# Performance work log

Measured on AMD Instinct MI355X. Metric: run time of the kernel, lower is better.

The kernel has to match this reference:

```python
import jax, jax.numpy as jnp
import numpy as np
import math

# ---- static configuration (mirrors Renderer defaults) ----
S = 129                                 # density cube side
L = math.ceil(S * math.sqrt(3))         # padded/rotation cube side = 224
C_ABS = 0.2                             # absorption coefficient c
LIGHTS = [
    {'dir': (2, 1, 1),    'rgb': (1.0, 69.0 / 255.0, 25.0 / 255.0)},
    {'dir': (-1, 0.5, 0), 'rgb': (227.0 / 255.0, 1.0, 66.0 / 255.0)},
]


def yp_from_light(l):
    ld = np.asarray(l, dtype=np.float64)
    ld = ld / np.sqrt(np.sum(ld ** 2))
    y = -math.asin(ld[0])
    if ld[2] < 0:
        y = -math.pi - y
    y = y * 180.0 / math.pi
    p = math.asin(ld[1]) * 180.0 / math.pi
    return y, p


def rot_matrix(yaw_deg, pitch_deg, order):
    # yaw about the y (height) axis, pitch about the x axis, roll = 0
    y = math.radians(yaw_deg)
    p = math.radians(pitch_deg)
    Ry = np.array([[math.cos(y), 0.0, math.sin(y)],
                   [0.0, 1.0, 0.0],
                   [-math.sin(y), 0.0, math.cos(y)]], dtype=np.float32)
    Rp = np.array([[1.0, 0.0, 0.0],
                   [0.0, math.cos(p), -math.sin(p)],
                   [0.0, math.sin(p), math.cos(p)]], dtype=np.float32)
    return Ry @ Rp if order == 'ypr' else Rp @ Ry

# base normalized sampling grid (align_corners=True convention), (x,y,z) order
_lin = np.linspace(-1.0, 1.0, L, dtype=np.float32)
_zz, _yy, _xx = np.meshgrid(_lin, _lin, _lin, indexing='ij')
BASE_XYZ = np.stack([_xx, _yy, _zz], axis=-1)   # [L,L,L,3]


def rotate_volume(vol, R):
    """Trilinear resampling of vol [B,C,D,H,W] under rotation R (zero padding)."""
    B, Ch, D, H, W = vol.shape
    src = jnp.einsum('dhwc,kc->dhwk', jnp.asarray(BASE_XYZ), jnp.asarray(R))
    xs = (src[..., 0] + 1.0) * 0.5 * (W - 1)
    ys = (src[..., 1] + 1.0) * 0.5 * (H - 1)
    zs = (src[..., 2] + 1.0) * 0.5 * (D - 1)
    x0 = jnp.floor(xs).astype(jnp.int32)
    y0 = jnp.floor(ys).astype(jnp.int32)
    z0 = jnp.floor(zs).astype(jnp.int32)
    wx = (xs - x0).astype(vol.dtype)
    wy = (ys - y0).astype(vol.dtype)
    wz = (zs - z0).astype(vol.dtype)
    flat = vol.reshape(B, Ch, D * H * W)

    def gather(zi, yi, xi):
        inb = ((zi >= 0) & (zi < D) & (yi >= 0) & (yi < H) & (xi >= 0) & (xi < W)).astype(vol.dtype)
        idx = ((jnp.clip(zi, 0, D - 1) * H + jnp.clip(yi, 0, H - 1)) * W
               + jnp.clip(xi, 0, W - 1)).reshape(-1)
        return jnp.take(flat, idx, axis=2).reshape(B, Ch, D, H, W) * inb

    out = (gather(z0,     y0,     x0)     * ((1 - wz) * (1 - wy) * (1 - wx))
         + gather(z0,     y0,     x0 + 1) * ((1 - wz) * (1 - wy) * wx)
         + gather(z0,     y0 + 1, x0)     * ((1 - wz) * wy * (1 - wx))
         + gather(z0,     y0 + 1, x0 + 1) * ((1 - wz) * wy * wx)
         + gather(z0 + 1, y0,     x0)     * (wz * (1 - wy) * (1 - wx))
         + gather(z0 + 1, y0,     x0 + 1) * (wz * (1 - wy) * wx)
         + gather(z0 + 1, y0 + 1, x0)     * (wz * wy * (1 - wx))
         + gather(z0 + 1, y0 + 1, x0 + 1) * (wz * wy * wx))
    return out


def _revcumsum(a):
    # torch.flip(cumsum(flip(a,[2]),2),[2]) : reverse cumulative sum along depth
    return jnp.flip(jnp.cumsum(jnp.flip(a, 2), axis=2), 2)


def setup_inputs() -> dict:
    key = jax.random.key(0)
    d = jax.random.uniform(key, (1, 1, S, S, S), dtype=jnp.float32)
    return {'d': d}


def reference(d):
    bs, _, Sd, _, _ = d.shape
    i = L // 2 - Sd // 2
    j = i + Sd
    light_array = jnp.zeros((bs, 3, Sd, Sd, Sd), dtype=d.dtype)
    for l in LIGHTS:
        y, p = yp_from_light(l['dir'])
        up = jnp.zeros((bs, 1, L, L, L), dtype=d.dtype).at[:, :, i:j, i:j, i:j].set(d)
        up = rotate_volume(up, rot_matrix(y, p, 'ypr'))
        up = jnp.exp(-C_ABS * _revcumsum(up))           # transmittance toward light
        up = rotate_volume(up, rot_matrix(-y, -p, 'rpy'))
        color = jnp.asarray(l['rgb'], dtype=d.dtype).reshape(1, 3, 1, 1, 1)
        light_array = light_array + up[:, :, i:j, i:j, i:j] * color
    t = jnp.exp(-C_ABS * _revcumsum(d))                  # view-ray transmittance
    out = C_ABS * jnp.sum(d * light_array * t, axis=2)   # background = 0
    return jnp.clip(out, 0.0, 1.0)
```

## Files before the change

kernel.cpp:

```cpp
#include <hip/hip_runtime.h>
#include <hip/hip_fp16.h>
#include <math.h>

#ifndef M_PI
#define M_PI 3.14159265358979323846
#endif

#define SS   129
#define LL   224
#define LL2  (LL*LL)
#define LL3  (LL*LL*LL)
#define SS2  (SS*SS)
#define SS3  (SS*SS*SS)
#define CABS 0.2f
#define PAD  48

#define BLO 45.5f
#define BHI 178.5f

#define NT1  28
#define NTZ16 14
#define ROTG  (2 * NTZ16 * 784)
#define NT3  17
#define NBZ16 9
#define BACKG (2 * NBZ16 * 289)
#define NTZ  28
#define NSEG 4
#define SEGZ 33
#define CVTB 8386

#define RBX 21
#define RBY 16
#define RBZ 18
#define RBN (RBX*RBY*RBZ)
#define RSXZ (RBX*RBZ)

#define BBX 21
#define BBY 16
#define BBZ 19
#define BBN (BBX*BBY*BBZ)
#define BSXZ (BBX*BBZ)

struct Mat3 { float m[9]; };
struct F3   { float x, y, z; };

__device__ __forceinline__ F3 tile_center(const Mat3& M, int ox, int oy, int oz) {
    float cbx = fmaf((float)ox + 3.5f, 2.0f / 223.0f, -1.0f);
    float cby = fmaf((float)oy + 3.5f, 2.0f / 223.0f, -1.0f);
    float cbz = fmaf((float)oz + 3.5f, 2.0f / 223.0f, -1.0f);
    F3 qc;
    qc.x = fmaf(fmaf(M.m[0], cbx, fmaf(M.m[1], cby, M.m[2] * cbz)), 111.5f, 111.5f);
    qc.y = fmaf(fmaf(M.m[3], cbx, fmaf(M.m[4], cby, M.m[5] * cbz)), 111.5f, 111.5f);
    qc.z = fmaf(fmaf(M.m[6], cbx, fmaf(M.m[7], cby, M.m[8] * cbz)), 111.5f, 111.5f);
    return qc;
}

__device__ __forceinline__ F3 tile_center16(const Mat3& M, int ox, int oy, int oz) {
    float cbx = fmaf((float)ox + 3.5f, 2.0f / 223.0f, -1.0f);
    float cby = fmaf((float)oy + 3.5f, 2.0f / 223.0f, -1.0f);
    float cbz = fmaf((float)oz + 7.5f, 2.0f / 223.0f, -1.0f);
    F3 qc;
    qc.x = fmaf(fmaf(M.m[0], cbx, fmaf(M.m[1], cby, M.m[2] * cbz)), 111.5f, 111.5f);
    qc.y = fmaf(fmaf(M.m[3], cbx, fmaf(M.m[4], cby, M.m[5] * cbz)), 111.5f, 111.5f);
    qc.z = fmaf(fmaf(M.m[6], cbx, fmaf(M.m[7], cby, M.m[8] * cbz)), 111.5f, 111.5f);
    return qc;
}

__device__ __forceinline__ bool tile_accept(F3 qc, F3 H) {
    return !(qc.x + H.x < BLO || qc.x - H.x > BHI ||
             qc.y + H.y < BLO || qc.y - H.y > BHI ||
             qc.z + H.z < BLO || qc.z - H.z > BHI);
}

__device__ __forceinline__ void qmap(const Mat3& M, int x, int y, int z,
                                     float& qx, float& qy, float& qz) {
    float bx = fmaf((float)x, 2.0f / 223.0f, -1.0f);
    float by = fmaf((float)y, 2.0f / 223.0f, -1.0f);
    float bz = fmaf((float)z, 2.0f / 223.0f, -1.0f);
    qx = fmaf(fmaf(M.m[0], bx, fmaf(M.m[1], by, M.m[2] * bz)), 111.5f, 111.5f);
    qy = fmaf(fmaf(M.m[3], bx, fmaf(M.m[4], by, M.m[5] * bz)), 111.5f, 111.5f);
    qz = fmaf(fmaf(M.m[6], bx, fmaf(M.m[7], by, M.m[8] * bz)), 111.5f, 111.5f);
}

__device__ __forceinline__ float fetch_d(const float* __restrict__ d, int z, int y, int x) {
    unsigned zz = (unsigned)(z - PAD), yy = (unsigned)(y - PAD), xx = (unsigned)(x - PAD);
    return (zz < (unsigned)SS && yy < (unsigned)SS && xx < (unsigned)SS)
        ? d[((int)zz * SS + (int)yy) * SS + (int)xx] : 0.0f;
}

__device__ __forceinline__ float fetch_d16(const __half* __restrict__ d, int z, int y, int x) {
    unsigned zz = (unsigned)(z - PAD), yy = (unsigned)(y - PAD), xx = (unsigned)(x - PAD);
    return (zz < (unsigned)SS && yy < (unsigned)SS && xx < (unsigned)SS)
        ? __half2float(d[((int)zz * SS + (int)yy) * SS + (int)xx]) : 0.0f;
}

__device__ __forceinline__ float fetch_T(const float* __restrict__ T, int z, int y, int x) {
    unsigned zz = (unsigned)z, yy = (unsigned)y, xx = (unsigned)x;
    return (zz < (unsigned)LL && yy < (unsigned)LL && xx < (unsigned)LL)
        ? T[((int)zz * LL + (int)yy) * LL + (int)xx] : 0.0f;
}

__device__ __forceinline__ float tri_T(const float* __restrict__ T, float qz, float qy, float qx) {
    int x0 = (int)floorf(qx), y0 = (int)floorf(qy), z0 = (int)floorf(qz);
    float wx = qx - (float)x0, wy = qy - (float)y0, wz = qz - (float)z0;
    float c000 = fetch_T(T, z0, y0, x0),     c001 = fetch_T(T, z0, y0, x0 + 1);
    float c010 = fetch_T(T, z0, y0 + 1, x0), c011 = fetch_T(T, z0, y0 + 1, x0 + 1);
    float c100 = fetch_T(T, z0 + 1, y0, x0),     c101 = fetch_T(T, z0 + 1, y0, x0 + 1);
    float c110 = fetch_T(T, z0 + 1, y0 + 1, x0), c111 = fetch_T(T, z0 + 1, y0 + 1, x0 + 1);
    float a00 = c000 + wx * (c001 - c000), a01 = c010 + wx * (c011 - c010);
    float a10 = c100 + wx * (c101 - c100), a11 = c110 + wx * (c111 - c110);
    float b0 = a00 + wy * (a01 - a00), b1 = a10 + wy * (a11 - a10);
    return b0 + wz * (b1 - b0);
}

__device__ __forceinline__ float tri_d_g(const float* __restrict__ d, float qz, float qy, float qx) {
    int x0 = (int)floorf(qx), y0 = (int)floorf(qy), z0 = (int)floorf(qz);
    float wx = qx - (float)x0, wy = qy - (float)y0, wz = qz - (float)z0;
    float c000 = fetch_d(d, z0, y0, x0),     c001 = fetch_d(d, z0, y0, x0 + 1);
    float c010 = fetch_d(d, z0, y0 + 1, x0), c011 = fetch_d(d, z0, y0 + 1, x0 + 1);
    float c100 = fetch_d(d, z0 + 1, y0, x0),     c101 = fetch_d(d, z0 + 1, y0, x0 + 1);
    float c110 = fetch_d(d, z0 + 1, y0 + 1, x0), c111 = fetch_d(d, z0 + 1, y0 + 1, x0 + 1);
    float a00 = c000 + wx * (c001 - c000), a01 = c010 + wx * (c011 - c010);
    float a10 = c100 + wx * (c101 - c100), a11 = c110 + wx * (c111 - c110);
    float b0 = a00 + wy * (a01 - a00), b1 = a10 + wy * (a11 - a10);
    return b0 + wz * (b1 - b0);
}

__device__ __forceinline__ float tri_rot(const float* __restrict__ S,
                                         float qx, float qy, float qz,
                                         int lox, int loy, int loz) {
    int x0 = (int)floorf(qx), y0 = (int)floorf(qy), z0 = (int)floorf(qz);
    float wx = qx - (float)x0, wy = qy - (float)y0, wz = qz - (float)z0;
    int i = (y0 - loy) * 378 + (z0 - loz) * 21 + (x0 - lox);
    float c000 = S[i],        c001 = S[i + 1];
    float cz0  = S[i + 21],   cz1  = S[i + 22];
    float cy0  = S[i + 378],  cy1  = S[i + 379];
    float cw0  = S[i + 399],  cw1  = S[i + 400];
    float a00 = c000 + wx * (c001 - c000);
    float a01 = cy0  + wx * (cy1  - cy0);
    float a10 = cz0  + wx * (cz1  - cz0);
    float a11 = cw0  + wx * (cw1  - cw0);
    float b0  = a00 + wy * (a01 - a00);
    float b1  = a10 + wy * (a11 - a10);
    return b0 + wz * (b1 - b0);
}

__device__ __forceinline__ float tri_back(const float* __restrict__ S,
                                          float qx, float qy, float qz,
                                          int lox, int loy, int loz) {
    int x0 = (int)floorf(qx), y0 = (int)floorf(qy), z0 = (int)floorf(qz);
    float wx = qx - (float)x0, wy = qy - (float)y0, wz = qz - (float)z0;
    int i = (y0 - loy) * 399 + (z0 - loz) * 21 + (x0 - lox);
    float c000 = S[i],        c001 = S[i + 1];
    float cz0  = S[i + 21],   cz1  = S[i + 22];
    float cy0  = S[i + 399],  cy1  = S[i + 400];
    float cw0  = S[i + 420],  cw1  = S[i + 421];
    float a00 = c000 + wx * (c001 - c000);
    float a01 = cy0  + wx * (cy1  - cy0);
    float a10 = cz0  + wx * (cz1  - cz0);
    float a11 = cw0  + wx * (cw1  - cw0);
    float b0  = a00 + wy * (a01 - a00);
    float b1  = a10 + wy * (a11 - a10);
    return b0 + wz * (b1 - b0);
}

__global__ __launch_bounds__(256) void k_pre(const float* __restrict__ d,
        float* __restrict__ Dseg, float* __restrict__ A,
        unsigned short* __restrict__ Run, __half* __restrict__ d16,
        Mat3 M0, Mat3 M1, F3 H0, F3 H1) {
    int b = blockIdx.x;
    if (b < 261) {
        int t = b * 256 + threadIdx.x;
        if (t < 2 * SS2) A[t] = 0.0f;
        if (t >= NSEG * SS2) return;
        int seg = t / SS2, col = t - seg * SS2;
        int zs = seg * SEGZ, ze = min(SS, zs + SEGZ);
        float run = 0.0f;
        for (int z = zs; z < ze; ++z) run += d[z * SS2 + col];
        Dseg[t] = run;
    } else if (b < 268) {
        int id = (b - 261) * 256 + threadIdx.x;
        if (id >= 2 * 784) return;
        int l = id / 784, r = id - l * 784;
        int ty = r / 28, tx = r - ty * 28;
        const Mat3 M = l ? M1 : M0;
        const F3  H  = l ? H1 : H0;
        int t0 = -1, t1 = -1;
        for (int tz = 0; tz < NT1; ++tz) {
            F3 qc = tile_center(M, tx * 8, ty * 8, tz * 8);
            if (tile_accept(qc, H)) { if (t0 < 0) t0 = tz; t1 = tz; }
        }
        Run[id] = (t0 < 0) ? 0xFFFFu : (unsigned short)(t0 | (t1 << 8));
    } else {
        int t = (b - 268) * 256 + threadIdx.x;
        if (t < SS3) d16[t] = __float2half(d[t]);
    }
}

__global__ __launch_bounds__(512) void k_rot(const __half* __restrict__ d16,
        __half* __restrict__ T0, __half* __restrict__ T1,
        float* __restrict__ S0, float* __restrict__ S1,
        const unsigned short* __restrict__ Run,
        Mat3 M0, Mat3 M1, F3 H0, F3 H1) {
    int b = blockIdx.x;
    int light = b / (NTZ16 * 784);
    int r = b - light * (NTZ16 * 784);
    int tz16 = r / 784;
    int r2 = r - tz16 * 784;
    int tty = r2 / 28, ttx = r2 - tty * 28;

    unsigned short rt = Run[light * 784 + tty * 28 + ttx];
    if (rt == 0xFFFFu) return;
    int t0 = rt & 0xFF, t1 = rt >> 8;
    if (2 * tz16 + 1 < t0 || 2 * tz16 > t1) return;

    const Mat3 M = light ? M1 : M0;
    const F3  H  = light ? H1 : H0;
    __half* __restrict__ T   = light ? T1 : T0;
    float* __restrict__ Ssum = light ? S1 : S0;

    int ox = ttx * 8, oy = tty * 8, oz = tz16 * 16;
    F3 qc = tile_center16(M, ox, oy, oz);

    int lox = (int)floorf(qc.x - H.x);
    int loy = (int)floorf(qc.y - H.y);
    int loz = (int)floorf(qc.z - H.z);

    __shared__ float S[RBN];
    __shared__ float Sc[1024];
    int tid = threadIdx.x;

    if (tid < RSXZ) {
        int ix = tid % RBX, iz = tid / RBX;
        bool interior = (lox >= PAD) & (lox <= PAD + SS - RBX) &
                        (loy >= PAD) & (loy <= PAD + SS - RBY) &
                        (loz >= PAD) & (loz <= PAD + SS - RBZ);
        if (interior) {
            const __half* g = d16 + ((size_t)(loz + iz - PAD) * SS + (loy - PAD)) * SS
                                  + (lox + ix - PAD);
            #pragma unroll
            for (int j = 0; j < RBY; ++j)
                S[tid + j * RSXZ] = __half2float(g[j * SS]);
        } else {
            #pragma unroll
            for (int j = 0; j < RBY; ++j)
                S[tid + j * RSXZ] = fetch_d16(d16, loz + iz, loy + j, lox + ix);
        }
    }
    __syncthreads();

    int lx = tid & 7, ly = (tid >> 3) & 7, lz = tid >> 6;
    int col = tid & 63;
    float fx = (float)lx - 3.5f, fy = (float)ly - 3.5f, fz = (float)lz - 7.5f;
    float qx = qc.x + fmaf(M.m[0], fx, fmaf(M.m[1], fy, M.m[2] * fz));
    float qy = qc.y + fmaf(M.m[3], fx, fmaf(M.m[4], fy, M.m[5] * fz));
    float qz = qc.z + fmaf(M.m[6], fx, fmaf(M.m[7], fy, M.m[8] * fz));
    float v0 = tri_rot(S, qx, qy, qz, lox, loy, loz);
    float qx2 = qx + 8.0f * M.m[2];
    float qy2 = qy + 8.0f * M.m[5];
    float qz2 = qz + 8.0f * M.m[8];
    float v1 = tri_rot(S, qx2, qy2, qz2, lox, loy, loz);

    Sc[lz * 64 + col] = v0;
    Sc[(lz + 8) * 64 + col] = v1;
    __syncthreads();
    if (tid < 64) {
        int so = (oy + (tid >> 3)) * LL + (ox + (tid & 7));
        float s = 0.0f;
        #pragma unroll
        for (int k = 15; k >= 8; --k) { s += Sc[k * 64 + tid]; Sc[k * 64 + tid] = s; }
        Ssum[(2 * tz16 + 1) * LL2 + so] = s;
        float s2 = 0.0f;
        #pragma unroll
        for (int k = 7; k >= 0; --k) { s2 += Sc[k * 64 + tid]; Sc[k * 64 + tid] = s2; }
        Ssum[(2 * tz16) * LL2 + so] = s2;
    }
    __syncthreads();
    int to = (oy + ly) * LL + (ox + lx);
    T[(size_t)(oz + lz) * LL2 + to]     = __float2half(Sc[lz * 64 + col]);
    T[(size_t)(oz + 8 + lz) * LL2 + to] = __float2half(Sc[(lz + 8) * 64 + col]);
}

__global__ __launch_bounds__(256) void k_sufw(float* __restrict__ S0,
        float* __restrict__ S1, const unsigned short* __restrict__ Run,
        const float* __restrict__ d, const float* __restrict__ Dseg,
        __half* __restrict__ W) {
    int b = blockIdx.x;
    if (b < 392) {
        int l = b / 196;
        int col = (b - l * 196) * 256 + threadIdx.x;
        float* __restrict__ Ssum = l ? S1 : S0;
        int x = col % LL, y = col / LL;
        unsigned short r = Run[l * 784 + (y >> 3) * 28 + (x >> 3)];
        if (r == 0xFFFFu) return;
        int t0 = r & 0xFF, t1 = r >> 8;
        float vbuf[NTZ];
        #pragma unroll
        for (int t = 0; t < NTZ; ++t)
            vbuf[t] = (t >= t0 && t <= t1) ? Ssum[t * LL2 + col] : 0.0f;
        float run = 0.0f;
        #pragma unroll
        for (int t = NTZ - 1; t >= 0; --t) {
            if (t >= t0 && t <= t1) Ssum[t * LL2 + col] = run;
            run += vbuf[t];
        }
    } else {
        int t = (b - 392) * 256 + threadIdx.x;
        if (t >= NSEG * SS2) return;
        int seg = t / SS2, col = t - seg * SS2;
        int zs = seg * SEGZ, ze = min(SS, zs + SEGZ);
        float run = 0.0f;
        for (int s2 = seg + 1; s2 < NSEG; ++s2) run += Dseg[s2 * SS2 + col];
        for (int z = ze - 1; z >= zs; --z) {
            float dv = d[z * SS2 + col];
            run += dv;
            W[z * SS2 + col] = __float2half(dv * __expf(-CABS * run));
        }
    }
}

template<bool BINT>
__global__ __launch_bounds__(512) void k_back(const __half* __restrict__ T0,
        const __half* __restrict__ T1, const float* __restrict__ S0,
        const float* __restrict__ S1, const __half* __restrict__ W,
        float* __restrict__ A0, float* __restrict__ A1,
        Mat3 M0, Mat3 M1, F3 H0, F3 H1) {
    int b = blockIdx.x;
    int light = b / (NBZ16 * 289); b -= light * (NBZ16 * 289);
    int tz16 = b / 289;
    int r2 = b - tz16 * 289;
    int tty = r2 / 17, ttx = r2 - tty * 17;

    const Mat3 M = light ? M1 : M0;
    const F3  H  = light ? H1 : H0;
    const __half* __restrict__ T   = light ? T1 : T0;
    const float* __restrict__ Ssum = light ? S1 : S0;
    float* __restrict__ A = light ? A1 : A0;

    int ox = ttx * 8, oy = tty * 8, oz = tz16 * 16;
    F3 qc = tile_center16(M, ox + PAD, oy + PAD, oz + PAD);
    int lox = (int)floorf(qc.x - H.x);
    int loy = (int)floorf(qc.y - H.y);
    int loz = (int)floorf(qc.z - H.z);

    __shared__ float S[BBN];
    __shared__ float Sc[1024];
    int tid = threadIdx.x;

    if (tid < BSXZ) {
        int ix = tid % BBX, iz = tid / BBX;
        if (BINT) {
            const __half* tb = T + ((size_t)(loz + iz) * LL + loy) * LL + (lox + ix);
            const float* sb = Ssum + (size_t)((loz + iz) >> 3) * LL2 + loy * LL + (lox + ix);
            #pragma unroll
            for (int j = 0; j < BBY; ++j)
                S[tid + j * BSXZ] = __expf(-CABS * (__half2float(tb[j * LL]) + sb[j * LL]));
        } else {
            #pragma unroll
            for (int j = 0; j < BBY; ++j) {
                int gz = loz + iz, gy = loy + j, gx = lox + ix;
                bool inb = ((unsigned)gz < (unsigned)LL) & ((unsigned)gy < (unsigned)LL)
                         & ((unsigned)gx < (unsigned)LL);
                float e = 0.0f;
                if (inb)
                    e = __expf(-CABS * (__half2float(T[((size_t)gz * LL + gy) * LL + gx])
                                      + Ssum[(size_t)(gz >> 3) * LL2 + gy * LL + gx]));
                S[tid + j * BSXZ] = e;
            }
        }
    }
    __syncthreads();

    int lx = tid & 7, ly = (tid >> 3) & 7, lz = tid >> 6;
    int col = tid & 63;
    int x = ox + lx, y = oy + ly;
    float v0 = 0.0f, v1 = 0.0f;
    if (x < SS && y < SS) {
        float fx = (float)lx - 3.5f, fy = (float)ly - 3.5f, fz = (float)lz - 7.5f;
        float qx = qc.x + fmaf(M.m[0], fx, fmaf(M.m[1], fy, M.m[2] * fz));
        float qy = qc.y + fmaf(M.m[3], fx, fmaf(M.m[4], fy, M.m[5] * fz));
        float qz = qc.z + fmaf(M.m[6], fx, fmaf(M.m[7], fy, M.m[8] * fz));
        int z0 = oz + lz, z1 = oz + 8 + lz;
        if (z0 < SS)
            v0 = tri_back(S, qx, qy, qz, lox, loy, loz)
               * __half2float(W[(z0 * SS + y) * SS + x]);
        if (z1 < SS) {
            float qx2 = qx + 8.0f * M.m[2];
            float qy2 = qy + 8.0f * M.m[5];
            float qz2 = qz + 8.0f * M.m[8];
            v1 = tri_back(S, qx2, qy2, qz2, lox, loy, loz)
               * __half2float(W[(z1 * SS + y) * SS + x]);
        }
    }
    Sc[lz * 64 + col] = v0;
    Sc[(lz + 8) * 64 + col] = v1;
    __syncthreads();
    if (tid < 64) {
        float s = 0.0f;
        #pragma unroll
        for (int k = 0; k < 16; ++k) s += Sc[k * 64 + tid];
        int xx = ox + (tid & 7), yy = oy + (tid >> 3);
        if (xx < SS && yy < SS) atomicAdd(&A[yy * SS + xx], s);
    }
}

__global__ __launch_bounds__(256) void k_combine(const float* __restrict__ A0,
        const float* __restrict__ A1, float* __restrict__ out, F3 c0, F3 c1) {
    int i = blockIdx.x * 256 + threadIdx.x;
    if (i >= 3 * SS2) return;
    int ch = i / SS2, col = i - ch * SS2;
    float r0 = (ch == 0) ? c0.x : ((ch == 1) ? c0.y : c0.z);
    float r1 = (ch == 0) ? c1.x : ((ch == 1) ? c1.y : c1.z);
    float o = CABS * (A0[col] * r0 + A1[col] * r1);
    out[i] = fminf(fmaxf(o, 0.0f), 1.0f);
}

__global__ __launch_bounds__(256) void k_rot_full(const float* __restrict__ d,
                                                  float* __restrict__ T, Mat3 R) {
    int i = blockIdx.x * 256 + threadIdx.x;
    if (i >= LL3) return;
    int x = i % LL; int r = i / LL; int y = r % LL; int z = r / LL;
    float qx, qy, qz; qmap(R, x, y, z, qx, qy, qz);
    T[i] = tri_d_g(d, qz, qy, qx);
}

__global__ __launch_bounds__(256) void k_scan_full(float* __restrict__ T) {
    int col = blockIdx.x * 256 + threadIdx.x;
    if (col >= LL2) return;
    float run = 0.0f;
    for (int z = LL - 1; z >= 0; --z) {
        int idx = z * LL2 + col;
        run += T[idx];
        T[idx] = __expf(-CABS * run);
    }
}

__global__ __launch_bounds__(64) void k_fused_back(const float* __restrict__ T,
        const float* __restrict__ d, float* __restrict__ LA, Mat3 RT,
        float cr, float cg, float cb, int first) {
    int col = blockIdx.x * 64 + threadIdx.x;
    if (col >= SS2) return;
    int y = col / SS, x = col % SS;
    float run = 0.0f, acc = 0.0f;
    for (int z = SS - 1; z >= 0; --z) {
        float qx, qy, qz; qmap(RT, x + PAD, y + PAD, z + PAD, qx, qy, qz);
        float u = tri_T(T, qz, qy, qx);
        float dv = d[z * SS2 + col];
        run += dv;
        acc = fmaf(dv * __expf(-CABS * run), u, acc);
    }
    if (first) {
        LA[0 * SS2 + col] = acc * cr;
        LA[1 * SS2 + col] = acc * cg;
        LA[2 * SS2 + col] = acc * cb;
    } else {
        LA[0 * SS2 + col] += acc * cr;
        LA[1 * SS2 + col] += acc * cg;
        LA[2 * SS2 + col] += acc * cb;
    }
}

__global__ __launch_bounds__(256) void k_clip(const float* __restrict__ LA,
                                              float* __restrict__ out) {
    int i = blockIdx.x * 256 + threadIdx.x;
    if (i < 3 * SS2) out[i] = fminf(fmaxf(CABS * LA[i], 0.0f), 1.0f);
}

static void light_mats(const double ld_in[3], Mat3& R, Mat3& RT) {
    double n = sqrt(ld_in[0]*ld_in[0] + ld_in[1]*ld_in[1] + ld_in[2]*ld_in[2]);
    double l0 = ld_in[0]/n, l1 = ld_in[1]/n, l2 = ld_in[2]/n;
    double yv = -asin(l0);
    if (l2 < 0) yv = -M_PI - yv;
    double yd = yv * 180.0 / M_PI, pd = asin(l1) * 180.0 / M_PI;
    double yr = yd * M_PI / 180.0, pr = pd * M_PI / 180.0;
    float cy = (float)cos(yr), sy = (float)sin(yr), cp = (float)cos(pr), sp = (float)sin(pr);
    float m[9] = { cy,  sy*sp,  sy*cp,
                   0.f, cp,    -sp,
                  -sy,  cy*sp,  cy*cp };
    for (int i = 0; i < 9; ++i) R.m[i] = m[i];
    RT.m[0] = m[0]; RT.m[1] = m[3]; RT.m[2] = m[6];
    RT.m[3] = m[1]; RT.m[4] = m[4]; RT.m[5] = m[7];
    RT.m[6] = m[2]; RT.m[7] = m[5]; RT.m[8] = m[8];
}

static F3 half_span8(const Mat3& M) {
    F3 h;
    h.x = 3.5f * (fabsf(M.m[0]) + fabsf(M.m[1]) + fabsf(M.m[2])) + 0.05f;
    h.y = 3.5f * (fabsf(M.m[3]) + fabsf(M.m[4]) + fabsf(M.m[5])) + 0.05f;
    h.z = 3.5f * (fabsf(M.m[6]) + fabsf(M.m[7]) + fabsf(M.m[8])) + 0.05f;
    return h;
}

static F3 half_span16(const Mat3& M) {
    F3 h;
    h.x = 3.5f * (fabsf(M.m[0]) + fabsf(M.m[1])) + 7.5f * fabsf(M.m[2]) + 0.1f;
    h.y = 3.5f * (fabsf(M.m[3]) + fabsf(M.m[4])) + 7.5f * fabsf(M.m[5]) + 0.1f;
    h.z = 3.5f * (fabsf(M.m[6]) + fabsf(M.m[7])) + 7.5f * fabsf(M.m[8]) + 0.1f;
    return h;
}

static void h_qc16(const Mat3& M, double ox, double oy, double oz, double q[3]) {
    double cb[3] = { (ox + 3.5) * 2.0 / 223.0 - 1.0,
                     (oy + 3.5) * 2.0 / 223.0 - 1.0,
                     (oz + 7.5) * 2.0 / 223.0 - 1.0 };
    for (int k = 0; k < 3; ++k)
        q[k] = ((double)M.m[3*k] * cb[0] + (double)M.m[3*k+1] * cb[1]
              + (double)M.m[3*k+2] * cb[2]) * 111.5 + 111.5;
}

extern "C" void kernel_launch(void* const* d_in, const int* in_sizes, int n_in,
                              void* d_out, int out_size, void* d_ws, size_t ws_size,
                              hipStream_t stream) {
    const float* d = (const float*)d_in[0];
    float* out = (float*)d_out;

    const double dirs[2][3] = { {2.0, 1.0, 1.0}, {-1.0, 0.5, 0.0} };
    F3 c0 = { 1.0f, 69.0f / 255.0f, 25.0f / 255.0f };
    F3 c1 = { 227.0f / 255.0f, 1.0f, 66.0f / 255.0f };
    Mat3 R[2], RT[2];
    light_mats(dirs[0], R[0], RT[0]);
    light_mats(dirs[1], R[1], RT[1]);
    F3 H8[2]  = { half_span8(R[0]),  half_span8(R[1])  };
    F3 H16[2] = { half_span16(R[0]), half_span16(R[1]) };
    F3 HB[2]  = { half_span16(RT[0]), half_span16(RT[1]) };

    bool bint = true;
    for (int l = 0; l < 2 && bint; ++l) {
        double H[3] = { HB[l].x, HB[l].y, HB[l].z };
        int dim[3] = { BBX, BBY, BBZ };
        for (int tz = 0; tz < NBZ16 && bint; ++tz)
            for (int ty = 0; ty < NT3 && bint; ++ty)
                for (int tx = 0; tx < NT3; ++tx) {
                    double q[3]; h_qc16(RT[l], tx * 8 + PAD, ty * 8 + PAD, tz * 16 + PAD, q);
                    for (int k = 0; k < 3; ++k) {
                        int lo = (int)floor(q[k] - H[k]);
                        if (lo < 1 || lo + dim[k] > LL - 1) { bint = false; break; }
                    }
                    if (!bint) break;
                }
    }

    const size_t f32n = (size_t)(2 * NTZ * LL2 + NSEG * SS2 + 2 * SS2);
    const size_t need_A = f32n * 4 + (size_t)(2 * SS3 + 2 * LL3) * 2 + 2 * 784 * 2;
    const size_t need_C = (size_t)(LL3 + 3 * SS2) * 4;

    if (ws_size >= need_A) {
        float* S0   = (float*)d_ws;
        float* S1   = S0 + NTZ * LL2;
        float* Dseg = S1 + NTZ * LL2;
        float* A0   = Dseg + NSEG * SS2;
        float* A1   = A0 + SS2;
        __half* W   = (__half*)(A1 + SS2);
        __half* d16 = W + SS3;
        __half* T0  = d16 + SS3;
        __half* T1  = T0 + LL3;
        unsigned short* Run = (unsigned short*)(T1 + LL3);

        k_pre  <<<268 + CVTB, 256, 0, stream>>>(d, Dseg, A0, Run, d16,
                                                R[0], R[1], H8[0], H8[1]);
        k_rot  <<<ROTG, 512, 0, stream>>>(d16, T0, T1, S0, S1, Run,
                                          R[0], R[1], H16[0], H16[1]);
        k_sufw <<<653, 256, 0, stream>>>(S0, S1, Run, d, Dseg, W);
        if (bint)
            k_back<true><<<BACKG, 512, 0, stream>>>(T0, T1, S0, S1, W, A0, A1,
                                                    RT[0], RT[1], HB[0], HB[1]);
        else
            k_back<false><<<BACKG, 512, 0, stream>>>(T0, T1, S0, S1, W, A0, A1,
                                                     RT[0], RT[1], HB[0], HB[1]);
        k_combine<<<(3 * SS2 + 255) / 256, 256, 0, stream>>>(A0, A1, out, c0, c1);
    } else if (ws_size >= need_C) {
        float* T  = (float*)d_ws;
        float* LA = T + LL3;
        for (int l = 0; l < 2; ++l) {
            k_rot_full <<<(LL3 + 255) / 256, 256, 0, stream>>>(d, T, R[l]);
            k_scan_full<<<(LL2 + 255) / 256, 256, 0, stream>>>(T);
            k_fused_back<<<(SS2 + 63) / 64, 64, 0, stream>>>(T, d, LA, RT[l],
                l ? c1.x : c0.x, l ? c1.y : c0.y, l ? c1.z : c0.z, l == 0);
        }
        k_clip<<<(3 * SS2 + 255) / 256, 256, 0, stream>>>(LA, out);
    }
}
```

Before: 177.5 us.

## Precompute transmittance in separate pass, vectorize conversion, finer scan segments

Adds a k_texp kernel that applies the suffix offset and the exp to the rotated half-precision volume once, in place, so k_back only loads ready transmittance values instead of recomputing exp plus an extra fp32 gather per staged voxel. Also raises the number of depth segments for the view-ray scan, vectorizes the fp32-to-half conversion with float4, splits the two tile scans across two warps, and makes W alias d16 to save workspace. The trade-off is an extra launch plus a full read-modify-write pass over the tile range, and W overwriting d16 depends on k_rot having finished with d16 before k_sufw writes, which stream ordering provides.

Measured after the change: 174.0 us. 2.0% less time.

```diff
diff --git a/kernel.cpp b/kernel.cpp
--- a/kernel.cpp
+++ b/kernel.cpp
@@ -25,9 +25,17 @@
 #define NBZ16 9
 #define BACKG (2 * NBZ16 * 289)
 #define NTZ  28
-#define NSEG 4
-#define SEGZ 33
-#define CVTB 8386
+
+#define NSEG 16
+#define SEGZ 9
+#define DSEGT (NSEG * SS2)
+#define PREB1 ((DSEGT + 255) / 256)
+#define PRERUNB 7
+#define N4   (SS3 / 4)
+#define CVT4B ((N4 + 1 + 255) / 256)
+#define PREG (PREB1 + PRERUNB + CVT4B)
+#define SUFG (392 + PREB1)
+#define TEXPB (2 * NTZ * LL2 / 256)
 
 #define RBX 21
 #define RBY 16
@@ -169,17 +177,17 @@
         unsigned short* __restrict__ Run, __half* __restrict__ d16,
         Mat3 M0, Mat3 M1, F3 H0, F3 H1) {
     int b = blockIdx.x;
-    if (b < 261) {
+    if (b < PREB1) {
         int t = b * 256 + threadIdx.x;
         if (t < 2 * SS2) A[t] = 0.0f;
-        if (t >= NSEG * SS2) return;
+        if (t >= DSEGT) return;
         int seg = t / SS2, col = t - seg * SS2;
         int zs = seg * SEGZ, ze = min(SS, zs + SEGZ);
         float run = 0.0f;
         for (int z = zs; z < ze; ++z) run += d[z * SS2 + col];
         Dseg[t] = run;
-    } else if (b < 268) {
-        int id = (b - 261) * 256 + threadIdx.x;
+    } else if (b < PREB1 + PRERUNB) {
+        int id = (b - PREB1) * 256 + threadIdx.x;
         if (id >= 2 * 784) return;
         int l = id / 784, r = id - l * 784;
         int ty = r / 28, tx = r - ty * 28;
@@ -192,8 +200,15 @@
         }
         Run[id] = (t0 < 0) ? 0xFFFFu : (unsigned short)(t0 | (t1 << 8));
     } else {
-        int t = (b - 268) * 256 + threadIdx.x;
-        if (t < SS3) d16[t] = __float2half(d[t]);
+        int t4 = (b - PREB1 - PRERUNB) * 256 + threadIdx.x;
+        if (t4 < N4) {
+            float4 v = ((const float4*)d)[t4];
+            __half2* o = (__half2*)(d16 + 4 * t4);
+            o[0] = __floats2half2_rn(v.x, v.y);
+            o[1] = __floats2half2_rn(v.z, v.w);
+        } else if (t4 == N4) {
+            d16[SS3 - 1] = __float2half(d[SS3 - 1]);
+        }
     }
 }
 
@@ -264,16 +279,20 @@
     Sc[lz * 64 + col] = v0;
     Sc[(lz + 8) * 64 + col] = v1;
     __syncthreads();
-    if (tid < 64) {
-        int so = (oy + (tid >> 3)) * LL + (ox + (tid & 7));
-        float s = 0.0f;
-        #pragma unroll
-        for (int k = 15; k >= 8; --k) { s += Sc[k * 64 + tid]; Sc[k * 64 + tid] = s; }
-        Ssum[(2 * tz16 + 1) * LL2 + so] = s;
-        float s2 = 0.0f;
-        #pragma unroll
-        for (int k = 7; k >= 0; --k) { s2 += Sc[k * 64 + tid]; Sc[k * 64 + tid] = s2; }
-        Ssum[(2 * tz16) * LL2 + so] = s2;
+    if (tid < 128) {
+        int c = tid & 63;
+        int so = (oy + (c >> 3)) * LL + (ox + (c & 7));
+        if (tid < 64) {
+            float s = 0.0f;
+            #pragma unroll
+            for (int k = 15; k >= 8; --k) { s += Sc[k * 64 + c]; Sc[k * 64 + c] = s; }
+            Ssum[(2 * tz16 + 1) * LL2 + so] = s;
+        } else {
+            float s2 = 0.0f;
+            #pragma unroll
+            for (int k = 7; k >= 0; --k) { s2 += Sc[k * 64 + c]; Sc[k * 64 + c] = s2; }
+            Ssum[(2 * tz16) * LL2 + so] = s2;
+        }
     }
     __syncthreads();
     int to = (oy + ly) * LL + (ox + lx);
@@ -306,7 +325,7 @@
         }
     } else {
         int t = (b - 392) * 256 + threadIdx.x;
-        if (t >= NSEG * SS2) return;
+        if (t >= DSEGT) return;
         int seg = t / SS2, col = t - seg * SS2;
         int zs = seg * SEGZ, ze = min(SS, zs + SEGZ);
         float run = 0.0f;
@@ -319,10 +338,32 @@
     }
 }
 
+__global__ __launch_bounds__(256) void k_texp(__half* __restrict__ T0,
+        __half* __restrict__ T1, const float* __restrict__ S0,
+        const float* __restrict__ S1, const unsigned short* __restrict__ Run) {
+    int id = blockIdx.x * 256 + threadIdx.x;
+    int light = id / (NTZ * LL2);
+    int r = id - light * (NTZ * LL2);
+    int t = r / LL2, col = r - t * LL2;
+    int y = col / LL, x = col - y * LL;
+    unsigned short rt = Run[light * 784 + (y >> 3) * 28 + (x >> 3)];
+    if (rt == 0xFFFFu) return;
+    int t0 = rt & 0xFF, t1 = rt >> 8;
+    if (t < t0 || t > t1) return;
+    const float* __restrict__ Ssum = light ? S1 : S0;
+    __half* __restrict__ T = light ? T1 : T0;
+    float off = Ssum[t * LL2 + col];
+    size_t base = (size_t)(8 * t) * LL2 + col;
+    #pragma unroll
+    for (int k = 0; k < 8; ++k) {
+        size_t idx = base + (size_t)k * LL2;
+        T[idx] = __float2half(__expf(-CABS * (__half2float(T[idx]) + off)));
+    }
+}
+
 template<bool BINT>
 __global__ __launch_bounds__(512) void k_back(const __half* __restrict__ T0,
-        const __half* __restrict__ T1, const float* __restrict__ S0,
-        const float* __restrict__ S1, const __half* __restrict__ W,
+        const __half* __restrict__ T1, const __half* __restrict__ W,
         float* __restrict__ A0, float* __restrict__ A1,
         Mat3 M0, Mat3 M1, F3 H0, F3 H1) {
     int b = blockIdx.x;
@@ -333,8 +374,7 @@
 
     const Mat3 M = light ? M1 : M0;
     const F3  H  = light ? H1 : H0;
-    const __half* __restrict__ T   = light ? T1 : T0;
-    const float* __restrict__ Ssum = light ? S1 : S0;
+    const __half* __restrict__ T = light ? T1 : T0;
     float* __restrict__ A = light ? A1 : A0;
 
     int ox = ttx * 8, oy = tty * 8, oz = tz16 * 16;
@@ -344,28 +384,24 @@
     int loz = (int)floorf(qc.z - H.z);
 
     __shared__ float S[BBN];
-    __shared__ float Sc[1024];
+    __shared__ float Sc[512];
     int tid = threadIdx.x;
 
     if (tid < BSXZ) {
         int ix = tid % BBX, iz = tid / BBX;
         if (BINT) {
             const __half* tb = T + ((size_t)(loz + iz) * LL + loy) * LL + (lox + ix);
-            const float* sb = Ssum + (size_t)((loz + iz) >> 3) * LL2 + loy * LL + (lox + ix);
             #pragma unroll
             for (int j = 0; j < BBY; ++j)
-                S[tid + j * BSXZ] = __expf(-CABS * (__half2float(tb[j * LL]) + sb[j * LL]));
+                S[tid + j * BSXZ] = __half2float(tb[j * LL]);
         } else {
             #pragma unroll
             for (int j = 0; j < BBY; ++j) {
                 int gz = loz + iz, gy = loy + j, gx = lox + ix;
                 bool inb = ((unsigned)gz < (unsigned)LL) & ((unsigned)gy < (unsigned)LL)
                          & ((unsigned)gx < (unsigned)LL);
-                float e = 0.0f;
-                if (inb)
-                    e = __expf(-CABS * (__half2float(T[((size_t)gz * LL + gy) * LL + gx])
-                                      + Ssum[(size_t)(gz >> 3) * LL2 + gy * LL + gx]));
-                S[tid + j * BSXZ] = e;
+                S[tid + j * BSXZ] = inb
+                    ? __half2float(T[((size_t)gz * LL + gy) * LL + gx]) : 0.0f;
             }
         }
     }
@@ -392,13 +428,12 @@
                * __half2float(W[(z1 * SS + y) * SS + x]);
         }
     }
-    Sc[lz * 64 + col] = v0;
-    Sc[(lz + 8) * 64 + col] = v1;
+    Sc[lz * 64 + col] = v0 + v1;
     __syncthreads();
     if (tid < 64) {
         float s = 0.0f;
         #pragma unroll
-        for (int k = 0; k < 16; ++k) s += Sc[k * 64 + tid];
+        for (int k = 0; k < 8; ++k) s += Sc[k * 64 + tid];
         int xx = ox + (tid & 7), yy = oy + (tid >> 3);
         if (xx < SS && yy < SS) atomicAdd(&A[yy * SS + xx], s);
     }
@@ -541,7 +576,7 @@
     }
 
     const size_t f32n = (size_t)(2 * NTZ * LL2 + NSEG * SS2 + 2 * SS2);
-    const size_t need_A = f32n * 4 + (size_t)(2 * SS3 + 2 * LL3) * 2 + 2 * 784 * 2;
+    const size_t need_A = f32n * 4 + (size_t)(SS3 + 2 * LL3) * 2 + 2 * 784 * 2;
     const size_t need_C = (size_t)(LL3 + 3 * SS2) * 4;
 
     if (ws_size >= need_A) {
@@ -550,22 +585,23 @@
         float* Dseg = S1 + NTZ * LL2;
         float* A0   = Dseg + NSEG * SS2;
         float* A1   = A0 + SS2;
-        __half* W   = (__half*)(A1 + SS2);
-        __half* d16 = W + SS3;
+        __half* d16 = (__half*)(A1 + SS2);
+        __half* W   = d16;
         __half* T0  = d16 + SS3;
         __half* T1  = T0 + LL3;
         unsigned short* Run = (unsigned short*)(T1 + LL3);
 
-        k_pre  <<<268 + CVTB, 256, 0, stream>>>(d, Dseg, A0, Run, d16,
-                                                R[0], R[1], H8[0], H8[1]);
+        k_pre  <<<PREG, 256, 0, stream>>>(d, Dseg, A0, Run, d16,
+                                          R[0], R[1], H8[0], H8[1]);
         k_rot  <<<ROTG, 512, 0, stream>>>(d16, T0, T1, S0, S1, Run,
                                           R[0], R[1], H16[0], H16[1]);
-        k_sufw <<<653, 256, 0, stream>>>(S0, S1, Run, d, Dseg, W);
+        k_sufw <<<SUFG, 256, 0, stream>>>(S0, S1, Run, d, Dseg, W);
+        k_texp <<<TEXPB, 256, 0, stream>>>(T0, T1, S0, S1, Run);
         if (bint)
-            k_back<true><<<BACKG, 512, 0, stream>>>(T0, T1, S0, S1, W, A0, A1,
+            k_back<true><<<BACKG, 512, 0, stream>>>(T0, T1, W, A0, A1,
                                                     RT[0], RT[1], HB[0], HB[1]);
         else
-            k_back<false><<<BACKG, 512, 0, stream>>>(T0, T1, S0, S1, W, A0, A1,
+            k_back<false><<<BACKG, 512, 0, stream>>>(T0, T1, W, A0, A1,
                                                      RT[0], RT[1], HB[0], HB[1]);
         k_combine<<<(3 * SS2 + 255) / 256, 256, 0, stream>>>(A0, A1, out, c0, c1);
     } else if (ws_size >= need_C) {
```
